# Kernel tuning notes

Measured on AMD Instinct MI355X. Metric: run time of the kernel, lower is better.

## Reference

```python
import jax, jax.numpy as jnp
import numpy as np

B, T, D_MODEL = 256, 200, 2048
D_KEY, D_VAL = 128, 128


def setup_inputs() -> dict:
    key = jax.random.key(0)
    k_q, k_mask, k_wq, k_wk, k_wv = jax.random.split(key, 5)
    q = jax.random.normal(k_q, (B, T, D_MODEL), dtype=jnp.float32)
    pad_mask = jax.random.randint(k_mask, (B, 1, T), 0, 2, dtype=jnp.int32)
    # ensure key 0 is never padded so every causal row has >=1 valid key (no NaN softmax)
    pad_mask = pad_mask.at[:, :, 0].set(0)
    s = 1.0 / np.sqrt(D_MODEL)
    Wq = jax.random.normal(k_wq, (D_KEY, D_MODEL), dtype=jnp.float32) * s
    Wk = jax.random.normal(k_wk, (D_KEY, D_MODEL), dtype=jnp.float32) * s
    Wv = jax.random.normal(k_wv, (D_VAL, D_MODEL), dtype=jnp.float32) * s
    return {"q": q, "pad_mask": pad_mask, "Wq": Wq, "Wk": Wk, "Wv": Wv}


def reference(q, pad_mask, Wq, Wk, Wv):
    # self-attention: kv = q
    T_ = q.shape[1]
    C = q.shape[-1]  # note: original scales by d_model, not d_key
    Q = jnp.einsum('btc,kc->btk', q, Wq)   # [B,T,d_key]
    K = jnp.einsum('btc,kc->btk', q, Wk)   # [B,T,d_key]
    V = jnp.einsum('btc,vc->btv', q, Wv)   # [B,T,d_val]
    W = jnp.einsum('bqk,btk->bqt', Q, K) / jnp.sqrt(jnp.asarray(C, q.dtype))  # [B,T,T]
    tril = jnp.tril(jnp.ones((T_, T_), dtype=jnp.bool_))
    neg_inf = jnp.asarray(-jnp.inf, W.dtype)
    W = jnp.where(tril[None, :, :], W, neg_inf)          # causal mask
    W = jnp.where(pad_mask == 1, neg_inf, W)             # padding mask (broadcast [B,1,T])
    W = jax.nn.softmax(W, axis=-1)
    # dropout p=0.0 / eval mode -> identity
    return jnp.einsum('bqt,btv->bqv', W, V)              # [B,T,d_val]
```

## Files before the change

### kernel.cpp

```cpp
#include <hip/hip_runtime.h>

typedef __bf16 bf16x8 __attribute__((ext_vector_type(8)));
typedef __bf16 bf16x4 __attribute__((ext_vector_type(4)));
typedef float  f32x4  __attribute__((ext_vector_type(4)));

#define MFMA16(a,b,c) __builtin_amdgcn_mfma_f32_16x16x32_bf16((a),(b),(c),0,0,0)

constexpr int B_ = 256, T_ = 200, DM = 2048, DK = 128;
constexpr int VT_STRIDE = 208;

constexpr size_t OFF_W = 0;
constexpr size_t OFF_Q = 1572864;
constexpr size_t OFF_K = OFF_Q + 13107200;
constexpr size_t OFF_V = OFF_K + 13107200;

__global__ __launch_bounds__(256) void wconv_kernel(const float* __restrict__ Wq,
                                                    const float* __restrict__ Wk,
                                                    const float* __restrict__ Wv,
                                                    __bf16* __restrict__ Wcat) {
  int idx = (blockIdx.x * 256 + threadIdx.x) * 4;
  int sel = idx >> 18;
  const float* base = (sel == 0) ? Wq : (sel == 1) ? Wk : Wv;
  float4 f = *(const float4*)(base + (idx - (sel << 18)));
  bf16x4 o;
  o[0] = (__bf16)f.x; o[1] = (__bf16)f.y; o[2] = (__bf16)f.z; o[3] = (__bf16)f.w;
  *(bf16x4*)(Wcat + idx) = o;
}

__global__ __launch_bounds__(512) void proj_kernel(const float* __restrict__ q,
                                                   const __bf16* __restrict__ Wcat,
                                                   __bf16* __restrict__ Qo,
                                                   __bf16* __restrict__ Ko,
                                                   __bf16* __restrict__ Vt) {
  __shared__ __bf16 sA[2][128][32];
  __shared__ __bf16 sB[2][384][32];

  const int tid  = threadIdx.x;
  const int lane = tid & 63;
  const int w    = tid >> 6;
  const int wm   = w >> 2, wn = w & 3;
  const int lhi  = lane >> 4, llo = lane & 15;
  const int m0   = blockIdx.x * 128;

  f32x4 acc[4][6];
#pragma unroll
  for (int i = 0; i < 4; ++i)
#pragma unroll
    for (int j = 0; j < 6; ++j) acc[i][j] = {0.f, 0.f, 0.f, 0.f};

  const int arow = tid >> 2, aseg = tid & 3;
  const float* aptr = q + (size_t)(m0 + arow) * DM + aseg * 8;
  int brow[3], bcol[3];
#pragma unroll
  for (int j = 0; j < 3; ++j) {
    int c = tid + j * 512;
    brow[j] = c >> 2; bcol[j] = (c & 3) * 8;
  }

  float4 fa0, fa1;
  bf16x8 fb[3];

#define ISSUE_LOADS(K0)                                                     \
  {                                                                         \
    const float4* s4 = (const float4*)(aptr + (K0));                        \
    fa0 = s4[0]; fa1 = s4[1];                                               \
    _Pragma("unroll")                                                       \
    for (int j = 0; j < 3; ++j)                                             \
      fb[j] = *(const bf16x8*)(Wcat + (size_t)brow[j] * DM + (K0) + bcol[j]); \
  }

#define WRITE_TILE(BUF)                                                     \
  {                                                                         \
    bf16x8 p;                                                               \
    p[0]=(__bf16)fa0.x; p[1]=(__bf16)fa0.y; p[2]=(__bf16)fa0.z; p[3]=(__bf16)fa0.w; \
    p[4]=(__bf16)fa1.x; p[5]=(__bf16)fa1.y; p[6]=(__bf16)fa1.z; p[7]=(__bf16)fa1.w; \
    *(bf16x8*)&sA[BUF][arow][aseg * 8] = p;                                 \
    _Pragma("unroll")                                                       \
    for (int j = 0; j < 3; ++j)                                             \
      *(bf16x8*)&sB[BUF][brow[j]][bcol[j]] = fb[j];                         \
  }

  constexpr int NK = DM / 32;
  ISSUE_LOADS(0);
  WRITE_TILE(0);
  __syncthreads();

  for (int it = 0; it < NK; ++it) {
    const int buf = it & 1;
    if (it + 1 < NK) ISSUE_LOADS((it + 1) * 32);

    bf16x8 af[4], bfr[6];
#pragma unroll
    for (int i = 0; i < 4; ++i) af[i]  = *(const bf16x8*)&sA[buf][wm * 64 + i * 16 + llo][lhi * 8];
#pragma unroll
    for (int j = 0; j < 6; ++j) bfr[j] = *(const bf16x8*)&sB[buf][wn * 96 + j * 16 + llo][lhi * 8];
#pragma unroll
    for (int i = 0; i < 4; ++i)
#pragma unroll
      for (int j = 0; j < 6; ++j) acc[i][j] = MFMA16(af[i], bfr[j], acc[i][j]);

    if (it + 1 < NK) WRITE_TILE(buf ^ 1);
    __syncthreads();
  }
#undef ISSUE_LOADS
#undef WRITE_TILE

#pragma unroll
  for (int i = 0; i < 4; ++i) {
#pragma unroll
    for (int r = 0; r < 4; ++r) {
      int row = m0 + wm * 64 + i * 16 + lhi * 4 + r;
      int b = row / 200;
      int t = row - b * 200;
#pragma unroll
      for (int j = 0; j < 6; ++j) {
        int col = wn * 96 + j * 16 + llo;
        __bf16 bv = (__bf16)acc[i][j][r];
        if (col < 128)       Qo[(size_t)row * DK + col] = bv;
        else if (col < 256)  Ko[(size_t)row * DK + (col - 128)] = bv;
        else                 Vt[((size_t)b * DK + (col - 256)) * VT_STRIDE + t] = bv;
      }
    }
  }
}

template <int QB>
__global__ __launch_bounds__(256, 1) void attn_kernel(const __bf16* __restrict__ Qg,
                                                      const __bf16* __restrict__ Kg,
                                                      const __bf16* __restrict__ Vt,
                                                      const int* __restrict__ padm,
                                                      float* __restrict__ out) {
  constexpr int Q0     = QB * 64;
  constexpr int KMAX   = (Q0 + 64 < T_) ? (Q0 + 64) : T_;
  constexpr int KTILES = (KMAX + 15) / 16;
  constexpr int KCC    = (KMAX + 31) / 32;
  constexpr int KT16   = KTILES * 16;
  constexpr int KP     = KCC * 32;
  constexpr int VS     = KP + 8;

  __shared__ __bf16 sK[KT16][136];
  __shared__ __bf16 sV[128][VS];
  __shared__ __bf16 sP[4][16][VS];
  __shared__ float  sMask[KT16];

  const int tid  = threadIdx.x;
  const int lane = tid & 63;
  const int w    = tid >> 6;
  const int b    = blockIdx.x;
  const int lhi  = lane >> 4, llo = lane & 15;

  for (int t = tid; t < KT16; t += 256) {
    float mv = -1e30f;
    if (t < KMAX && padm[b * T_ + t] == 0) mv = 0.0f;
    sMask[t] = mv;
  }
  for (int cid = tid; cid < KT16 * 16; cid += 256) {
    int t = cid >> 4, c = (cid & 15) * 8;
    int tg = (t < T_) ? t : (T_ - 1);
    *(bf16x8*)&sK[t][c] = *(const bf16x8*)(Kg + ((size_t)b * T_ + tg) * DK + c);
  }
  {
    constexpr int NCH = KP / 8;
    for (int cid = tid; cid < 128 * NCH; cid += 256) {
      int v = cid / NCH, t0 = (cid % NCH) * 8;
      bf16x8 val;
      if (t0 < VT_STRIDE) {
        val = *(const bf16x8*)(Vt + ((size_t)b * DK + v) * VT_STRIDE + t0);
      } else {
#pragma unroll
        for (int jz = 0; jz < 8; ++jz) val[jz] = (__bf16)0.0f;
      }
      *(bf16x8*)&sV[v][t0] = val;
    }
  }
  if constexpr (KT16 < KP) {
    constexpr int NC = (KP - KT16) / 8;
    for (int idx = tid; idx < 4 * 16 * NC; idx += 256) {
      int ww = idx / (16 * NC);
      int rem = idx % (16 * NC);
      int row = rem / NC, cc = (rem % NC) * 8;
      bf16x8 z;
#pragma unroll
      for (int jz = 0; jz < 8; ++jz) z[jz] = (__bf16)0.0f;
      *(bf16x8*)&sP[ww][row][KT16 + cc] = z;
    }
  }
  __syncthreads();

  const int q0w = Q0 + w * 16;
  bf16x8 qf[4];
  {
    int qrow = q0w + llo;
    if (qrow > T_ - 1) qrow = T_ - 1;
    const __bf16* qp = Qg + ((size_t)b * T_ + qrow) * DK + lhi * 8;
#pragma unroll
    for (int kk = 0; kk < 4; ++kk) qf[kk] = *(const bf16x8*)(qp + kk * 32);
  }

  float sc[KTILES][4];
  const float scale = 0.022097086912079608f;
#pragma unroll
  for (int tt = 0; tt < KTILES; ++tt) {
    f32x4 s = {0.f, 0.f, 0.f, 0.f};
    const __bf16* kp = &sK[tt * 16 + llo][lhi * 8];
#pragma unroll
    for (int kk = 0; kk < 4; ++kk) {
      bf16x8 kf = *(const bf16x8*)(kp + kk * 32);
      s = MFMA16(qf[kk], kf, s);
    }
    const int t = tt * 16 + llo;
    const float madd = sMask[t];
#pragma unroll
    for (int r = 0; r < 4; ++r) {
      int qq = q0w + lhi * 4 + r;
      float v = fmaf(s[r], scale, madd);
      sc[tt][r] = (t > qq) ? -1e30f : v;
    }
  }

#pragma unroll
  for (int r = 0; r < 4; ++r) {
    float mm = -3e38f;
#pragma unroll
    for (int tt = 0; tt < KTILES; ++tt) mm = fmaxf(mm, sc[tt][r]);
#pragma unroll
    for (int off = 1; off < 16; off <<= 1) mm = fmaxf(mm, __shfl_xor(mm, off));
    float ss = 0.f;
#pragma unroll
    for (int tt = 0; tt < KTILES; ++tt) { float e = __expf(sc[tt][r] - mm); sc[tt][r] = e; ss += e; }
#pragma unroll
    for (int off = 1; off < 16; off <<= 1) ss += __shfl_xor(ss, off);
    float inv = 1.0f / ss;
#pragma unroll
    for (int tt = 0; tt < KTILES; ++tt) sc[tt][r] *= inv;
  }

#pragma unroll
  for (int tt = 0; tt < KTILES; ++tt) {
    int t = tt * 16 + llo;
#pragma unroll
    for (int r = 0; r < 4; ++r) sP[w][lhi * 4 + r][t] = (__bf16)sc[tt][r];
  }
  __syncthreads();

  f32x4 oacc[8];
#pragma unroll
  for (int vt = 0; vt < 8; ++vt) oacc[vt] = {0.f, 0.f, 0.f, 0.f};
#pragma unroll
  for (int kc = 0; kc < KCC; ++kc) {
    bf16x8 pa = *(const bf16x8*)&sP[w][llo][kc * 32 + lhi * 8];
#pragma unroll
    for (int vt = 0; vt < 8; ++vt) {
      bf16x8 vb = *(const bf16x8*)&sV[vt * 16 + llo][kc * 32 + lhi * 8];
      oacc[vt] = MFMA16(pa, vb, oacc[vt]);
    }
  }

#pragma unroll
  for (int vt = 0; vt < 8; ++vt) {
#pragma unroll
    for (int r = 0; r < 4; ++r) {
      int qq = q0w + lhi * 4 + r;
      if (qq < T_) out[((size_t)b * T_ + qq) * DK + vt * 16 + llo] = oacc[vt][r];
    }
  }
}

extern "C" void kernel_launch(void* const* d_in, const int* in_sizes, int n_in,
                              void* d_out, int out_size, void* d_ws, size_t ws_size,
                              hipStream_t stream) {
  const float* q    = (const float*)d_in[0];
  const int*   padm = (const int*)d_in[1];
  const float* Wq   = (const float*)d_in[2];
  const float* Wk   = (const float*)d_in[3];
  const float* Wv   = (const float*)d_in[4];
  float* out        = (float*)d_out;

  char* ws = (char*)d_ws;
  __bf16* Wcat = (__bf16*)(ws + OFF_W);
  __bf16* Qb   = (__bf16*)(ws + OFF_Q);
  __bf16* Kb   = (__bf16*)(ws + OFF_K);
  __bf16* Vtb  = (__bf16*)(ws + OFF_V);

  wconv_kernel<<<768, 256, 0, stream>>>(Wq, Wk, Wv, Wcat);
  proj_kernel<<<400, 512, 0, stream>>>(q, Wcat, Qb, Kb, Vtb);
  attn_kernel<0><<<256, 256, 0, stream>>>(Qb, Kb, Vtb, padm, out);
  attn_kernel<1><<<256, 256, 0, stream>>>(Qb, Kb, Vtb, padm, out);
  attn_kernel<2><<<256, 256, 0, stream>>>(Qb, Kb, Vtb, padm, out);
  attn_kernel<3><<<256, 256, 0, stream>>>(Qb, Kb, Vtb, padm, out);
}
```

Measured before the change: 269.1 us.

## Deepen global-load prefetch to four stages in projection GEMM

The QKV projection GEMM now keeps four K-tiles of global loads in flight in registers instead of one, rotating through register sets while LDS stays double-buffered. It also replaces __syncthreads with a custom barrier that waits only on LDS counters, so outstanding global loads are not drained at each barrier. This is meant to hide global memory latency, at the cost of more registers per thread and a possible drop in occupancy.

```diff
diff --git a/kernel.cpp b/kernel.cpp
--- a/kernel.cpp
+++ b/kernel.cpp
@@ -57,53 +57,84 @@
     brow[j] = c >> 2; bcol[j] = (c & 3) * 8;
   }
 
-  float4 fa0, fa1;
-  bf16x8 fb[3];
-
-#define ISSUE_LOADS(K0)                                                     \
+  float4 a0x, a0y, a1x, a1y, a2x, a2y, a3x, a3y;
+  bf16x8 b0[3], b1[3], b2[3], b3[3];
+
+#define ISSUE(A0, A1, BB, K0)                                               \
   {                                                                         \
     const float4* s4 = (const float4*)(aptr + (K0));                        \
-    fa0 = s4[0]; fa1 = s4[1];                                               \
+    A0 = s4[0]; A1 = s4[1];                                                 \
     _Pragma("unroll")                                                       \
     for (int j = 0; j < 3; ++j)                                             \
-      fb[j] = *(const bf16x8*)(Wcat + (size_t)brow[j] * DM + (K0) + bcol[j]); \
-  }
-
-#define WRITE_TILE(BUF)                                                     \
+      BB[j] = *(const bf16x8*)(Wcat + (size_t)brow[j] * DM + (K0) + bcol[j]); \
+  }
+
+#define WRITETILE(A0, A1, BB, BUF)                                          \
   {                                                                         \
     bf16x8 p;                                                               \
-    p[0]=(__bf16)fa0.x; p[1]=(__bf16)fa0.y; p[2]=(__bf16)fa0.z; p[3]=(__bf16)fa0.w; \
-    p[4]=(__bf16)fa1.x; p[5]=(__bf16)fa1.y; p[6]=(__bf16)fa1.z; p[7]=(__bf16)fa1.w; \
+    p[0]=(__bf16)A0.x; p[1]=(__bf16)A0.y; p[2]=(__bf16)A0.z; p[3]=(__bf16)A0.w; \
+    p[4]=(__bf16)A1.x; p[5]=(__bf16)A1.y; p[6]=(__bf16)A1.z; p[7]=(__bf16)A1.w; \
     *(bf16x8*)&sA[BUF][arow][aseg * 8] = p;                                 \
     _Pragma("unroll")                                                       \
     for (int j = 0; j < 3; ++j)                                             \
-      *(bf16x8*)&sB[BUF][brow[j]][bcol[j]] = fb[j];                         \
-  }
-
-  constexpr int NK = DM / 32;
-  ISSUE_LOADS(0);
-  WRITE_TILE(0);
-  __syncthreads();
-
-  for (int it = 0; it < NK; ++it) {
-    const int buf = it & 1;
-    if (it + 1 < NK) ISSUE_LOADS((it + 1) * 32);
-
-    bf16x8 af[4], bfr[6];
-#pragma unroll
-    for (int i = 0; i < 4; ++i) af[i]  = *(const bf16x8*)&sA[buf][wm * 64 + i * 16 + llo][lhi * 8];
-#pragma unroll
-    for (int j = 0; j < 6; ++j) bfr[j] = *(const bf16x8*)&sB[buf][wn * 96 + j * 16 + llo][lhi * 8];
-#pragma unroll
-    for (int i = 0; i < 4; ++i)
-#pragma unroll
-      for (int j = 0; j < 6; ++j) acc[i][j] = MFMA16(af[i], bfr[j], acc[i][j]);
-
-    if (it + 1 < NK) WRITE_TILE(buf ^ 1);
-    __syncthreads();
-  }
-#undef ISSUE_LOADS
-#undef WRITE_TILE
+      *(bf16x8*)&sB[BUF][brow[j]][bcol[j]] = BB[j];                         \
+  }
+
+#define COMPUTE(BUF)                                                        \
+  {                                                                         \
+    bf16x8 af[4], bfr[6];                                                   \
+    _Pragma("unroll")                                                       \
+    for (int i = 0; i < 4; ++i) af[i]  = *(const bf16x8*)&sA[BUF][wm * 64 + i * 16 + llo][lhi * 8]; \
+    _Pragma("unroll")                                                       \
+    for (int j = 0; j < 6; ++j) bfr[j] = *(const bf16x8*)&sB[BUF][wn * 96 + j * 16 + llo][lhi * 8]; \
+    _Pragma("unroll")                                                       \
+    for (int i = 0; i < 4; ++i)                                             \
+      _Pragma("unroll")                                                     \
+      for (int j = 0; j < 6; ++j) acc[i][j] = MFMA16(af[i], bfr[j], acc[i][j]); \
+  }
+
+#define BAR()                                                               \
+  {                                                                         \
+    asm volatile("s_waitcnt lgkmcnt(0)" ::: "memory");                      \
+    __builtin_amdgcn_s_barrier();                                           \
+    asm volatile("" ::: "memory");                                          \
+  }
+
+  ISSUE(a0x, a0y, b0, 0);
+  ISSUE(a1x, a1y, b1, 32);
+  ISSUE(a2x, a2y, b2, 64);
+  ISSUE(a3x, a3y, b3, 96);
+  WRITETILE(a0x, a0y, b0, 0);
+  BAR();
+
+  for (int it = 0; it < 15; ++it) {
+    const int t0 = it * 4;
+    ISSUE(a0x, a0y, b0, (t0 + 4) * 32);
+    COMPUTE(0);
+    WRITETILE(a1x, a1y, b1, 1);
+    BAR();
+    ISSUE(a1x, a1y, b1, (t0 + 5) * 32);
+    COMPUTE(1);
+    WRITETILE(a2x, a2y, b2, 0);
+    BAR();
+    ISSUE(a2x, a2y, b2, (t0 + 6) * 32);
+    COMPUTE(0);
+    WRITETILE(a3x, a3y, b3, 1);
+    BAR();
+    ISSUE(a3x, a3y, b3, (t0 + 7) * 32);
+    COMPUTE(1);
+    WRITETILE(a0x, a0y, b0, 0);
+    BAR();
+  }
+  COMPUTE(0); WRITETILE(a1x, a1y, b1, 1); BAR();
+  COMPUTE(1); WRITETILE(a2x, a2y, b2, 0); BAR();
+  COMPUTE(0); WRITETILE(a3x, a3y, b3, 1); BAR();
+  COMPUTE(1);
+
+#undef ISSUE
+#undef WRITETILE
+#undef COMPUTE
+#undef BAR
 
 #pragma unroll
   for (int i = 0; i < 4; ++i) {
```

Result: faster. 251.8 us (-6.4%).
